# Kernel optimization log

Hardware: AMD Instinct MI355X
Metric: run time of the kernel (lower is better)

Reference implementation:

```python
import jax, jax.numpy as jnp
import numpy as np

PATCH = 3
SIGMA2 = 0.5 ** 2
EPS = 1e-8


def _gauss_kernel():
    # depthwise Gaussian patch kernel, shape (6, 1, P, P, P), normalized to sum 1
    c = (PATCH - 1) / 2.0
    zz, yy, xx = np.meshgrid(np.arange(PATCH), np.arange(PATCH), np.arange(PATCH), indexing='ij')
    d2 = (xx - c) ** 2 + (yy - c) ** 2 + (zz - c) ** 2
    g = np.exp(-d2 / SIGMA2).astype(np.float32)
    g /= g.sum()
    k = np.zeros((6, 1, PATCH, PATCH, PATCH), np.float32)
    k[:, 0] = g
    return jnp.asarray(k)


def _shift(x, axis, step):
    # zero-padded shift: step=+1 -> out[i] = x[i+1]; step=-1 -> out[i] = x[i-1]
    n = x.shape[axis]
    pad = [(0, 0)] * x.ndim
    lo = 1 if step > 0 else 0
    pad[axis] = (0, 1) if step > 0 else (1, 0)
    xp = jnp.pad(x, pad)
    idx = [slice(None)] * x.ndim
    idx[axis] = slice(lo, lo + n)
    return xp[tuple(idx)]


def _mind(img):
    # shift-conv (one-hot 3x3x3 kernels) == 6 axis shifts: +z,-z,+y,-y,+x,-x
    shifted = jnp.concatenate([
        _shift(img, 2, 1), _shift(img, 2, -1),
        _shift(img, 3, 1), _shift(img, 3, -1),
        _shift(img, 4, 1), _shift(img, 4, -1),
    ], axis=1)                                  # (B,6,D,H,W)
    diff2 = (shifted - img) ** 2                # broadcast over channel dim
    gk = _gauss_kernel()
    Dp = jax.lax.conv_general_dilated(
        diff2, gk, window_strides=(1, 1, 1), padding='SAME',
        feature_group_count=6,
        dimension_numbers=('NCDHW', 'OIDHW', 'NCDHW'))  # depthwise Gaussian smoothing
    Vx = Dp.mean(axis=1, keepdims=True)
    num = jnp.exp(-Dp / (Vx + EPS))
    return num / (num.sum(axis=1, keepdims=True) + EPS)


def setup_inputs() -> dict:
    key = jax.random.key(0)
    img = jax.random.normal(key, (2, 1, 192, 192, 192), dtype=jnp.float32)
    return {"img": img}


def reference(img):
    return _mind(img)
```

## Files before the change

### kernel.cpp

```cpp
#include <hip/hip_runtime.h>

#define DHW   192
#define DHW2  (DHW*DHW)
#define TX    64
#define TTY   4
#define YB    4
#define BY    (TTY*YB)
#define ZCH   8
#define NT    (TX*TTY)
#define RY    (BY+4)
#define RXW   (TX+8)
#define SLICE (RY*RXW)
#define NF4   (SLICE/4)
#define ROWF4 (RXW/4)

__device__ __forceinline__ void soft_barrier() {
    asm volatile("s_waitcnt lgkmcnt(0)" ::: "memory");
    __builtin_amdgcn_s_barrier();
    asm volatile("" ::: "memory");
}

__global__ __launch_bounds__(NT, 4)
void mind3d_kernel(const float* __restrict__ img, float* __restrict__ out)
{
    __shared__ float ring[4][SLICE];

    const int lane = threadIdx.x;
    const int ty   = threadIdx.y;
    const int tid  = ty*TX + lane;

    const int x0 = blockIdx.x * TX;
    const int y0 = blockIdx.y * BY;
    const int zi = blockIdx.z;
    const int nzc = DHW / ZCH;
    const int b  = zi / nzc;
    const int z0 = (zi - b*nzc) * ZCH;

    const float* imgb = img + (size_t)b * ((size_t)DHW * DHW2);

    const float a1 = 0.01831563889245986f;
    const float n1 = 1.0f/(1.0f + 2.0f*a1);
    const float norm3 = n1*n1*n1;

    const int gx = x0 + lane;
    const float mL = (gx == 0)     ? 0.f : 1.f;
    const float mR = (gx == DHW-1) ? 0.f : 1.f;
    const int wy = y0 + ty*YB;
    const int u  = lane + 4;

    const int r0  = tid / ROWF4, c0i = tid - r0*ROWF4;
    const int gy0s = y0 - 2 + r0, gx0s = x0 - 4 + (c0i << 2);
    const bool in0 = ((unsigned)gy0s < (unsigned)DHW) && ((unsigned)gx0s <= (unsigned)(DHW-4));
    const int t2  = tid + NT;
    const bool g2 = (t2 < NF4);
    const int r1  = t2 / ROWF4, c1i = t2 - r1*ROWF4;
    const int gy1s = y0 - 2 + r1, gx1s = x0 - 4 + (c1i << 2);
    const bool in1 = g2 && ((unsigned)gy1s < (unsigned)DHW) && ((unsigned)gx1s <= (unsigned)(DHW-4));

    float4 sv0, sv1;
    auto issue = [&](int z) {
        sv0 = float4{0.f,0.f,0.f,0.f};
        sv1 = float4{0.f,0.f,0.f,0.f};
        if ((unsigned)z < (unsigned)DHW) {
            const float* sp = imgb + (size_t)z * DHW2;
            if (in0) sv0 = *(const float4*)(sp + (size_t)gy0s*DHW + gx0s);
            if (in1) sv1 = *(const float4*)(sp + (size_t)gy1s*DHW + gx1s);
        }
    };
    auto commit = [&](int z) {
        float4* dst = (float4*)ring[(z + 8) & 3];
        dst[tid] = sv0;
        if (g2) dst[t2] = sv1;
    };

    float zm[YB][6], zc[YB][6], zS0[YB];
    #pragma unroll
    for (int j = 0; j < YB; ++j) {
        zS0[j] = 0.f;
        #pragma unroll
        for (int c = 0; c < 6; ++c) { zm[j][c] = 0.f; zc[j][c] = 0.f; }
    }

    issue(z0-2); commit(z0-2);
    issue(z0-1); commit(z0-1);
    issue(z0);   commit(z0);
    issue(z0+1);
    soft_barrier();

    for (int zs = z0 - 1; zs <= z0 + ZCH; ++zs) {
        if (zs + 2 <= z0 + ZCH + 1) commit(zs + 2);
        if (zs + 3 <= z0 + ZCH + 1) issue(zs + 3);

        const bool zok  = ((unsigned)zs < (unsigned)DHW);
        const bool warm = (zs == z0 - 1);
        const float* rcs = ring[(zs + 8) & 3] + ty*YB*RXW + u;
        const float* rps = ring[(zs + 9) & 3] + (ty*YB + 1)*RXW + u;
        const float* rms = ring[(zs + 7) & 3] + (ty*YB + 1)*RXW + u;

        float A1 = rcs[-1], A2 = rcs[0], A3 = rcs[1];
        float B0 = rcs[RXW-2], B1 = rcs[RXW-1], B2 = rcs[RXW], B3 = rcs[RXW+1], B4 = rcs[RXW+2];

        float T[3][6];
        const int zcout = zs - 1;
        const bool emitz = (zcout >= z0);

        #pragma unroll
        for (int k = 0; k < 6; ++k) {
            const int gr = wy - 1 + k;
            const float* rk = rcs + (k + 2)*RXW;
            float C0 = rk[-2], C1 = rk[-1], C2 = rk[0], C3 = rk[1], C4 = rk[2];
            const float* pk = rps + k*RXW;
            float zpL = pk[-1], zpC = pk[0], zpR = pk[1];

            const bool rowok = ((unsigned)gr < (unsigned)DHW);
            const bool rok   = zok && rowok;
            float* Tk = T[k % 3];

            {
                float eL = zpL-B1, eC = zpC-B2, eR = zpR-B3;
                Tk[0] = rowok ? (a1*(eL*eL*mL + eR*eR*mR) + eC*eC) : 0.f;
            }
            if (rok) {
                float d0 = B1-B0, d1 = B2-B1, d2 = B3-B2, d3 = B4-B3;
                float q0 = d0*d0, q1 = d1*d1, q2 = d2*d2, q3 = d3*d3;
                float eL, eC, eR;
                eL = C1-B1;  eC = C2-B2;  eR = C3-B3;
                Tk[2] = a1*(eL*eL*mL + eR*eR*mR) + eC*eC;
                eL = A1-B1;  eC = A2-B2;  eR = A3-B3;
                Tk[3] = a1*(eL*eL*mL + eR*eR*mR) + eC*eC;
                Tk[4] = a1*(q1*mL + q3*mR) + q2;
                Tk[5] = a1*(q0*mL + q2*mR) + q1;
            } else {
                Tk[2]=0.f; Tk[3]=0.f; Tk[4]=0.f; Tk[5]=0.f;
            }
            if (warm) {
                float t1v = 0.f;
                if (rok) {
                    const float* mk = rms + k*RXW;
                    float zmL = mk[-1], zmC = mk[0], zmR = mk[1];
                    float eL = zmL-B1, eC = zmC-B2, eR = zmR-B3;
                    t1v = a1*(eL*eL*mL + eR*eR*mR) + eC*eC;
                }
                Tk[1] = t1v;
            }

            if (k >= 2) {
                const int j = k - 2;
                float s0 = a1*(T[(k-2)%3][0] + T[k%3][0]) + T[(k-1)%3][0];
                float s2 = a1*(T[(k-2)%3][2] + T[k%3][2]) + T[(k-1)%3][2];
                float s3 = a1*(T[(k-2)%3][3] + T[k%3][3]) + T[(k-1)%3][3];
                float s4 = a1*(T[(k-2)%3][4] + T[k%3][4]) + T[(k-1)%3][4];
                float s5 = a1*(T[(k-2)%3][5] + T[k%3][5]) + T[(k-1)%3][5];
                float s1 = warm ? (a1*(T[(k-2)%3][1] + T[k%3][1]) + T[(k-1)%3][1])
                                : (zok ? zS0[j] : 0.f);
                zS0[j] = s0;
                float s0st = zok ? s0 : 0.f;
                float sp_[6] = {s0st, s1, s2, s3, s4, s5};

                if (emitz) {
                    float dp[6], sum = 0.f;
                    #pragma unroll
                    for (int c = 0; c < 6; ++c) {
                        dp[c] = norm3 * (a1*(zm[j][c] + sp_[c]) + zc[j][c]);
                        sum += dp[c];
                    }
                    float inv = 1.0f / (sum * (1.0f/6.0f) + 1e-8f);
                    float num[6], nsum = 0.f;
                    #pragma unroll
                    for (int c = 0; c < 6; ++c) {
                        num[c] = __expf(-dp[c] * inv);
                        nsum += num[c];
                    }
                    float rs = 1.0f / (nsum + 1e-8f);
                    size_t base = ((size_t)(6*b)*DHW + zcout) * (size_t)DHW2
                                + (size_t)(wy + j)*DHW + (size_t)gx;
                    #pragma unroll
                    for (int c = 0; c < 6; ++c)
                        out[base + (size_t)c * ((size_t)DHW*DHW2)] = num[c]*rs;
                }
                #pragma unroll
                for (int c = 0; c < 6; ++c) { zm[j][c] = zc[j][c]; zc[j][c] = sp_[c]; }
            }
            A1=B1; A2=B2; A3=B3;
            B0=C0; B1=C1; B2=C2; B3=C3; B4=C4;
        }
        soft_barrier();
    }
}

extern "C" void kernel_launch(void* const* d_in, const int* in_sizes, int n_in,
                              void* d_out, int out_size, void* d_ws, size_t ws_size,
                              hipStream_t stream)
{
    const float* img = (const float*)d_in[0];
    float* out = (float*)d_out;
    dim3 block(TX, TTY, 1);
    dim3 grid(DHW/TX, DHW/BY, 2*(DHW/ZCH));
    hipLaunchKernelGGL(mind3d_kernel, grid, block, 0, stream, img, out);
}
```

Before: 410.7 us.

## Remap threads to 4 x-outputs per thread with float4 LDS loads and stores

Each thread now computes four consecutive x outputs on a single y row, where before it computed one x column over four y rows. Shared-memory reads become float4 loads of three adjacent vectors per row, and the six output channels are written as float4 stores. The aim is fewer LDS instructions and wider global stores for this memory-bound kernel. In exchange, each thread recomputes the y-direction 3-tap sums across three rows instead of sliding them, register pressure rises, and launch bounds drop to 3 waves.

```diff
diff --git a/kernel.cpp b/kernel.cpp
--- a/kernel.cpp
+++ b/kernel.cpp
@@ -2,14 +2,10 @@
 
 #define DHW   192
 #define DHW2  (DHW*DHW)
-#define TX    64
-#define TTY   4
-#define YB    4
-#define BY    (TTY*YB)
 #define ZCH   8
-#define NT    (TX*TTY)
-#define RY    (BY+4)
-#define RXW   (TX+8)
+#define NT    256
+#define RY    20
+#define RXW   72
 #define SLICE (RY*RXW)
 #define NF4   (SLICE/4)
 #define ROWF4 (RXW/4)
@@ -20,17 +16,20 @@
     asm volatile("" ::: "memory");
 }
 
-__global__ __launch_bounds__(NT, 4)
+__global__ __launch_bounds__(NT, 3)
 void mind3d_kernel(const float* __restrict__ img, float* __restrict__ out)
 {
-    __shared__ float ring[4][SLICE];
+    __shared__ __align__(16) float ring[4][SLICE];
 
     const int lane = threadIdx.x;
-    const int ty   = threadIdx.y;
-    const int tid  = ty*TX + lane;
-
-    const int x0 = blockIdx.x * TX;
-    const int y0 = blockIdx.y * BY;
+    const int wid  = threadIdx.y;
+    const int tid  = wid*64 + lane;
+
+    const int xq   = lane & 15;
+    const int yrow = wid*4 + (lane >> 4);
+
+    const int x0 = blockIdx.x * 64;
+    const int y0 = blockIdx.y * 16;
     const int zi = blockIdx.z;
     const int nzc = DHW / ZCH;
     const int b  = zi / nzc;
@@ -42,11 +41,15 @@
     const float n1 = 1.0f/(1.0f + 2.0f*a1);
     const float norm3 = n1*n1*n1;
 
-    const int gx = x0 + lane;
-    const float mL = (gx == 0)     ? 0.f : 1.f;
-    const float mR = (gx == DHW-1) ? 0.f : 1.f;
-    const int wy = y0 + ty*YB;
-    const int u  = lane + 4;
+    const int bx  = x0 + xq*4;
+    const int gyo = y0 + yrow;
+
+    const float cl0 = (bx == 0)         ? 0.f : a1;
+    const float cr3 = (bx + 3 == DHW-1) ? 0.f : a1;
+    const float cl[4] = {cl0, a1, a1, a1};
+    const float cr[4] = {a1, a1, a1, cr3};
+    const float myA = (gyo == 0)     ? 0.f : a1;
+    const float myC = (gyo == DHW-1) ? 0.f : a1;
 
     const int r0  = tid / ROWF4, c0i = tid - r0*ROWF4;
     const int gy0s = y0 - 2 + r0, gx0s = x0 - 4 + (c0i << 2);
@@ -73,9 +76,9 @@
         if (g2) dst[t2] = sv1;
     };
 
-    float zm[YB][6], zc[YB][6], zS0[YB];
+    float zm[4][6], zc[4][6], zS0[4];
     #pragma unroll
-    for (int j = 0; j < YB; ++j) {
+    for (int j = 0; j < 4; ++j) {
         zS0[j] = 0.f;
         #pragma unroll
         for (int c = 0; c < 6; ++c) { zm[j][c] = 0.f; zc[j][c] = 0.f; }
@@ -87,102 +90,119 @@
     issue(z0+1);
     soft_barrier();
 
+    const int qb = 1 + xq;
+
     for (int zs = z0 - 1; zs <= z0 + ZCH; ++zs) {
         if (zs + 2 <= z0 + ZCH + 1) commit(zs + 2);
         if (zs + 3 <= z0 + ZCH + 1) issue(zs + 3);
 
         const bool zok  = ((unsigned)zs < (unsigned)DHW);
         const bool warm = (zs == z0 - 1);
-        const float* rcs = ring[(zs + 8) & 3] + ty*YB*RXW + u;
-        const float* rps = ring[(zs + 9) & 3] + (ty*YB + 1)*RXW + u;
-        const float* rms = ring[(zs + 7) & 3] + (ty*YB + 1)*RXW + u;
-
-        float A1 = rcs[-1], A2 = rcs[0], A3 = rcs[1];
-        float B0 = rcs[RXW-2], B1 = rcs[RXW-1], B2 = rcs[RXW], B3 = rcs[RXW+1], B4 = rcs[RXW+2];
-
-        float T[3][6];
+        const float4* c4 = (const float4*)ring[(zs + 8) & 3];
+        const float4* p4 = (const float4*)ring[(zs + 9) & 3];
+        const float4* m4 = (const float4*)ring[(zs + 7) & 3];
+
+        auto ld8 = [&](const float4* s4, int r, float* w) {
+            float4 A = s4[r*ROWF4 + qb - 1];
+            float4 B = s4[r*ROWF4 + qb];
+            float4 C = s4[r*ROWF4 + qb + 1];
+            w[0]=A.z; w[1]=A.w; w[2]=B.x; w[3]=B.y;
+            w[4]=B.z; w[5]=B.w; w[6]=C.x; w[7]=C.y;
+        };
+
+        float SS[6][4];
+        #pragma unroll
+        for (int c = 0; c < 6; ++c)
+            #pragma unroll
+            for (int j = 0; j < 4; ++j) SS[c][j] = 0.f;
+
+        auto dorow = [&](const float* RA, const float* RB, const float* RC,
+                         const float* P, float cy) {
+            float q[7];
+            #pragma unroll
+            for (int i = 0; i < 7; ++i) { float d = RB[i+1]-RB[i]; q[i] = d*d; }
+            float E0[6], E2[6], E3[6];
+            #pragma unroll
+            for (int i = 0; i < 6; ++i) {
+                float e;
+                e = P[i+1]  - RB[i+1]; E0[i] = e*e;
+                e = RC[i+1] - RB[i+1]; E2[i] = e*e;
+                e = RA[i+1] - RB[i+1]; E3[i] = e*e;
+            }
+            #pragma unroll
+            for (int j = 0; j < 4; ++j) {
+                float t;
+                t = cl[j]*E0[j] + (cr[j]*E0[j+2] + E0[j+1]); SS[0][j] += cy*t;
+                t = cl[j]*E2[j] + (cr[j]*E2[j+2] + E2[j+1]); SS[2][j] += cy*t;
+                t = cl[j]*E3[j] + (cr[j]*E3[j+2] + E3[j+1]); SS[3][j] += cy*t;
+                t = cl[j]*q[j+1] + (cr[j]*q[j+3] + q[j+2]);  SS[4][j] += cy*t;
+                t = cl[j]*q[j]   + (cr[j]*q[j+2] + q[j+1]);  SS[5][j] += cy*t;
+            }
+        };
+        auto dorow1 = [&](const float* RB, const float* PM, float cy) {
+            float E1[6];
+            #pragma unroll
+            for (int i = 0; i < 6; ++i) { float e = PM[i+1]-RB[i+1]; E1[i] = e*e; }
+            #pragma unroll
+            for (int j = 0; j < 4; ++j) {
+                float t = cl[j]*E1[j] + (cr[j]*E1[j+2] + E1[j+1]);
+                SS[1][j] += cy*t;
+            }
+        };
+
+        float L0[8],L1[8],L2[8],L3[8],L4[8],P[8];
+        ld8(c4, yrow+0, L0);
+        ld8(c4, yrow+1, L1);
+        ld8(c4, yrow+2, L2);
+        ld8(p4, yrow+1, P);
+        dorow(L0, L1, L2, P, myA);
+        if (warm) { float PM[8]; ld8(m4, yrow+1, PM); dorow1(L1, PM, myA); }
+        ld8(c4, yrow+3, L3);
+        ld8(p4, yrow+2, P);
+        dorow(L1, L2, L3, P, 1.f);
+        if (warm) { float PM[8]; ld8(m4, yrow+2, PM); dorow1(L2, PM, 1.f); }
+        ld8(c4, yrow+4, L4);
+        ld8(p4, yrow+3, P);
+        dorow(L2, L3, L4, P, myC);
+        if (warm) { float PM[8]; ld8(m4, yrow+3, PM); dorow1(L3, PM, myC); }
+
         const int zcout = zs - 1;
         const bool emitz = (zcout >= z0);
-
+        float o[6][4];
         #pragma unroll
-        for (int k = 0; k < 6; ++k) {
-            const int gr = wy - 1 + k;
-            const float* rk = rcs + (k + 2)*RXW;
-            float C0 = rk[-2], C1 = rk[-1], C2 = rk[0], C3 = rk[1], C4 = rk[2];
-            const float* pk = rps + k*RXW;
-            float zpL = pk[-1], zpC = pk[0], zpR = pk[1];
-
-            const bool rowok = ((unsigned)gr < (unsigned)DHW);
-            const bool rok   = zok && rowok;
-            float* Tk = T[k % 3];
-
-            {
-                float eL = zpL-B1, eC = zpC-B2, eR = zpR-B3;
-                Tk[0] = rowok ? (a1*(eL*eL*mL + eR*eR*mR) + eC*eC) : 0.f;
-            }
-            if (rok) {
-                float d0 = B1-B0, d1 = B2-B1, d2 = B3-B2, d3 = B4-B3;
-                float q0 = d0*d0, q1 = d1*d1, q2 = d2*d2, q3 = d3*d3;
-                float eL, eC, eR;
-                eL = C1-B1;  eC = C2-B2;  eR = C3-B3;
-                Tk[2] = a1*(eL*eL*mL + eR*eR*mR) + eC*eC;
-                eL = A1-B1;  eC = A2-B2;  eR = A3-B3;
-                Tk[3] = a1*(eL*eL*mL + eR*eR*mR) + eC*eC;
-                Tk[4] = a1*(q1*mL + q3*mR) + q2;
-                Tk[5] = a1*(q0*mL + q2*mR) + q1;
-            } else {
-                Tk[2]=0.f; Tk[3]=0.f; Tk[4]=0.f; Tk[5]=0.f;
-            }
-            if (warm) {
-                float t1v = 0.f;
-                if (rok) {
-                    const float* mk = rms + k*RXW;
-                    float zmL = mk[-1], zmC = mk[0], zmR = mk[1];
-                    float eL = zmL-B1, eC = zmC-B2, eR = zmR-B3;
-                    t1v = a1*(eL*eL*mL + eR*eR*mR) + eC*eC;
+        for (int j = 0; j < 4; ++j) {
+            float s0 = SS[0][j];
+            float s1 = warm ? SS[1][j] : (zok ? zS0[j] : 0.f);
+            zS0[j] = s0;
+            float s0st = zok ? s0 : 0.f;
+            float sp[6] = {s0st, s1, SS[2][j], SS[3][j], SS[4][j], SS[5][j]};
+
+            if (emitz) {
+                float dp[6], sum = 0.f;
+                #pragma unroll
+                for (int c = 0; c < 6; ++c) {
+                    dp[c] = norm3 * (a1*(zm[j][c] + sp[c]) + zc[j][c]);
+                    sum += dp[c];
                 }
-                Tk[1] = t1v;
-            }
-
-            if (k >= 2) {
-                const int j = k - 2;
-                float s0 = a1*(T[(k-2)%3][0] + T[k%3][0]) + T[(k-1)%3][0];
-                float s2 = a1*(T[(k-2)%3][2] + T[k%3][2]) + T[(k-1)%3][2];
-                float s3 = a1*(T[(k-2)%3][3] + T[k%3][3]) + T[(k-1)%3][3];
-                float s4 = a1*(T[(k-2)%3][4] + T[k%3][4]) + T[(k-1)%3][4];
-                float s5 = a1*(T[(k-2)%3][5] + T[k%3][5]) + T[(k-1)%3][5];
-                float s1 = warm ? (a1*(T[(k-2)%3][1] + T[k%3][1]) + T[(k-1)%3][1])
-                                : (zok ? zS0[j] : 0.f);
-                zS0[j] = s0;
-                float s0st = zok ? s0 : 0.f;
-                float sp_[6] = {s0st, s1, s2, s3, s4, s5};
-
-                if (emitz) {
-                    float dp[6], sum = 0.f;
-                    #pragma unroll
-                    for (int c = 0; c < 6; ++c) {
-                        dp[c] = norm3 * (a1*(zm[j][c] + sp_[c]) + zc[j][c]);
-                        sum += dp[c];
-                    }
-                    float inv = 1.0f / (sum * (1.0f/6.0f) + 1e-8f);
-                    float num[6], nsum = 0.f;
-                    #pragma unroll
-                    for (int c = 0; c < 6; ++c) {
-                        num[c] = __expf(-dp[c] * inv);
-                        nsum += num[c];
-                    }
-                    float rs = 1.0f / (nsum + 1e-8f);
-                    size_t base = ((size_t)(6*b)*DHW + zcout) * (size_t)DHW2
-                                + (size_t)(wy + j)*DHW + (size_t)gx;
-                    #pragma unroll
-                    for (int c = 0; c < 6; ++c)
-                        out[base + (size_t)c * ((size_t)DHW*DHW2)] = num[c]*rs;
-                }
+                float inv = 1.0f / (sum * (1.0f/6.0f) + 1e-8f);
+                float num[6], nsum = 0.f;
                 #pragma unroll
-                for (int c = 0; c < 6; ++c) { zm[j][c] = zc[j][c]; zc[j][c] = sp_[c]; }
-            }
-            A1=B1; A2=B2; A3=B3;
-            B0=C0; B1=C1; B2=C2; B3=C3; B4=C4;
+                for (int c = 0; c < 6; ++c) { num[c] = __expf(-dp[c]*inv); nsum += num[c]; }
+                float rs = 1.0f / (nsum + 1e-8f);
+                #pragma unroll
+                for (int c = 0; c < 6; ++c) o[c][j] = num[c]*rs;
+            }
+            #pragma unroll
+            for (int c = 0; c < 6; ++c) { zm[j][c] = zc[j][c]; zc[j][c] = sp[c]; }
+        }
+        if (emitz) {
+            size_t base = ((size_t)(6*b)*DHW + zcout)*(size_t)DHW2
+                        + (size_t)gyo*DHW + (size_t)bx;
+            #pragma unroll
+            for (int c = 0; c < 6; ++c) {
+                float4 v = {o[c][0], o[c][1], o[c][2], o[c][3]};
+                *(float4*)(&out[base + (size_t)c*((size_t)DHW*DHW2)]) = v;
+            }
         }
         soft_barrier();
     }
@@ -194,7 +214,7 @@
 {
     const float* img = (const float*)d_in[0];
     float* out = (float*)d_out;
-    dim3 block(TX, TTY, 1);
-    dim3 grid(DHW/TX, DHW/BY, 2*(DHW/ZCH));
+    dim3 block(64, 4, 1);
+    dim3 grid(DHW/64, DHW/16, 2*(DHW/ZCH));
     hipLaunchKernelGGL(mind3d_kernel, grid, block, 0, stream, img, out);
 }
```

Result: slower. 567.2 us (+38.1%).
